# Performance work log

Measured on AMD Instinct MI355X. Metric: run time of the kernel, lower is better.

## Reference

```python
import jax, jax.numpy as jnp
import numpy as np
from jax import lax

FACTOR = 2  # downsample factor


def make_resample_kernel(k):
    k = np.asarray(k, dtype=np.float32)
    if k.ndim == 1:
        k = np.outer(k, k)
    k /= k.sum()
    return jnp.asarray(k)


def setup_inputs() -> dict:
    key = jax.random.key(0)
    x = jax.random.normal(key, (16, 512, 64, 64), dtype=jnp.float32)
    kernel = make_resample_kernel([1, 3, 3, 1])  # (4, 4), normalized binomial FIR
    return {"x": x, "kernel": kernel}


def reference(x, kernel):
    # upfirdn2d(x, kernel, up=1, down=factor, pad=((kh-factor+1)//2, (kh-factor)//2))
    # = pad -> correlate with flipped kernel (i.e. true convolution) -> stride-`factor` subsample.
    # Fused here as a single depthwise strided conv.
    n, c, h, w = x.shape
    kh, kw = kernel.shape
    pad = kh - FACTOR
    pad0, pad1 = (pad + 1) // 2, pad // 2
    wk = jnp.flip(kernel, (0, 1))[None, None]          # (1, 1, kh, kw)
    wk = jnp.broadcast_to(wk, (c, 1, kh, kw))          # depthwise kernel
    out = lax.conv_general_dilated(
        x, wk,
        window_strides=(FACTOR, FACTOR),
        padding=((pad0, pad1), (pad0, pad1)),
        dimension_numbers=("NCHW", "OIHW", "NCHW"),
        feature_group_count=c,
    )  # (n, c, h//FACTOR, w//FACTOR)
    return out
```

## Files before the change

### kernel.cpp

```cpp
#include <hip/hip_runtime.h>


#define IH 64
#define IW 64
#define OHN 32
#define OWN 32
#define HP 33

__global__ __launch_bounds__(256) void upfirdn_down2_kernel(
    const float* __restrict__ x, const float* __restrict__ kk,
    float* __restrict__ out)
{
    __shared__ float hbuf[IH * HP];

    const int t = threadIdx.x;
    const int img = blockIdx.x;
    const float* __restrict__ xi = x + (size_t)img * (IH * IW);
    float* __restrict__ oi = out + (size_t)img * (OHN * OWN);

    float km[16];
#pragma unroll
    for (int i = 0; i < 16; ++i) km[i] = kk[i];
    const float kh0 = km[3] + km[7] + km[11] + km[15];
    const float kh1 = km[2] + km[6] + km[10] + km[14];
    const float kh2 = km[1] + km[5] + km[9]  + km[13];
    const float kh3 = km[0] + km[4] + km[8]  + km[12];
    const float kv0 = km[12] + km[13] + km[14] + km[15];
    const float kv1 = km[8]  + km[9]  + km[10] + km[11];
    const float kv2 = km[4]  + km[5]  + km[6]  + km[7];
    const float kv3 = km[0]  + km[1]  + km[2]  + km[3];

    {
        const int y = t >> 2;
        const int q = t & 3;
        const float* row = xi + y * IW + q * 16;
        const float4 a0 = ((const float4*)row)[0];
        const float4 a1 = ((const float4*)row)[1];
        const float4 a2 = ((const float4*)row)[2];
        const float4 a3 = ((const float4*)row)[3];
        const float left  = (q > 0) ? row[-1] : 0.0f;
        const float right = (q < 3) ? row[16] : 0.0f;

        float v[18];
        v[0] = left;
        v[1] = a0.x;  v[2] = a0.y;  v[3] = a0.z;  v[4] = a0.w;
        v[5] = a1.x;  v[6] = a1.y;  v[7] = a1.z;  v[8] = a1.w;
        v[9] = a2.x;  v[10] = a2.y; v[11] = a2.z; v[12] = a2.w;
        v[13] = a3.x; v[14] = a3.y; v[15] = a3.z; v[16] = a3.w;
        v[17] = right;

        float* hb = &hbuf[y * HP + q * 8];
#pragma unroll
        for (int m = 0; m < 8; ++m) {
            hb[m] = kh0 * v[2 * m] + kh1 * v[2 * m + 1]
                  + kh2 * v[2 * m + 2] + kh3 * v[2 * m + 3];
        }
    }
    __syncthreads();

    {
        const int ow = t & 31;
        const int g = t >> 5;
        const int ybase = 8 * g - 1;
        float hr[10];
#pragma unroll
        for (int r = 0; r < 10; ++r) {
            const int yy = ybase + r;
            hr[r] = (yy >= 0 && yy < IH) ? hbuf[yy * HP + ow] : 0.0f;
        }
#pragma unroll
        for (int m = 0; m < 4; ++m) {
            const float o = kv0 * hr[2 * m] + kv1 * hr[2 * m + 1]
                          + kv2 * hr[2 * m + 2] + kv3 * hr[2 * m + 3];
            oi[(4 * g + m) * OWN + ow] = o;
        }
    }
}

extern "C" void kernel_launch(void* const* d_in, const int* in_sizes, int n_in,
                              void* d_out, int out_size, void* d_ws, size_t ws_size,
                              hipStream_t stream) {
    const float* x = (const float*)d_in[0];
    const float* k = (const float*)d_in[1];
    float* out = (float*)d_out;
    const int n_img = in_sizes[0] / (IH * IW);
    upfirdn_down2_kernel<<<n_img, 256, 0, stream>>>(x, k, out);
}
```

Baseline: 196.2 us.

## Coalesce input loads with lane shuffles and vectorize LDS and output accesses

Each thread now loads one float4 per iteration in a fully coalesced pattern, taking its left and right neighbours from adjacent lanes with shuffles instead of issuing separate scalar loads. The horizontal-pass buffer gains zero-padded top and bottom rows and a 36-float pitch, so the vertical pass can read four float4 rows from LDS without bounds checks and write float4 outputs. The aim is to cut uncoalesced global loads and scalar LDS and store traffic in this memory-bound kernel. Relying on shuffles assumes 16-lane row groups stay inside a wavefront, and the new pitch may change LDS bank-conflict behaviour.

Result: no change. 196.9 us (+0.3%).

```diff
diff --git a/kernel.cpp b/kernel.cpp
--- a/kernel.cpp
+++ b/kernel.cpp
@@ -5,75 +5,66 @@
 #define IW 64
 #define OHN 32
 #define OWN 32
-#define HP 33
+#define HP 36
+#define HROWS 66
 
 __global__ __launch_bounds__(256) void upfirdn_down2_kernel(
     const float* __restrict__ x, const float* __restrict__ kk,
     float* __restrict__ out)
 {
-    __shared__ float hbuf[IH * HP];
+    __shared__ float hbuf[HROWS * HP];
 
     const int t = threadIdx.x;
     const int img = blockIdx.x;
     const float* __restrict__ xi = x + (size_t)img * (IH * IW);
     float* __restrict__ oi = out + (size_t)img * (OHN * OWN);
 
-    float km[16];
+    if (t < HP) hbuf[t] = 0.0f;
+    else if (t < 2 * HP) hbuf[(HROWS - 1) * HP + (t - HP)] = 0.0f;
+
+    const float4 k0 = ((const float4*)kk)[0];
+    const float4 k1 = ((const float4*)kk)[1];
+    const float4 k2 = ((const float4*)kk)[2];
+    const float4 k3 = ((const float4*)kk)[3];
+    const float kh0 = k0.w + k1.w + k2.w + k3.w;
+    const float kh1 = k0.z + k1.z + k2.z + k3.z;
+    const float kh2 = k0.y + k1.y + k2.y + k3.y;
+    const float kh3 = k0.x + k1.x + k2.x + k3.x;
+    const float kv0 = k3.x + k3.y + k3.z + k3.w;
+    const float kv1 = k2.x + k2.y + k2.z + k2.w;
+    const float kv2 = k1.x + k1.y + k1.z + k1.w;
+    const float kv3 = k0.x + k0.y + k0.z + k0.w;
+
+    const int c4 = t & 15;
+    const int rb = t >> 4;
 #pragma unroll
-    for (int i = 0; i < 16; ++i) km[i] = kk[i];
-    const float kh0 = km[3] + km[7] + km[11] + km[15];
-    const float kh1 = km[2] + km[6] + km[10] + km[14];
-    const float kh2 = km[1] + km[5] + km[9]  + km[13];
-    const float kh3 = km[0] + km[4] + km[8]  + km[12];
-    const float kv0 = km[12] + km[13] + km[14] + km[15];
-    const float kv1 = km[8]  + km[9]  + km[10] + km[11];
-    const float kv2 = km[4]  + km[5]  + km[6]  + km[7];
-    const float kv3 = km[0]  + km[1]  + km[2]  + km[3];
-
-    {
-        const int y = t >> 2;
-        const int q = t & 3;
-        const float* row = xi + y * IW + q * 16;
-        const float4 a0 = ((const float4*)row)[0];
-        const float4 a1 = ((const float4*)row)[1];
-        const float4 a2 = ((const float4*)row)[2];
-        const float4 a3 = ((const float4*)row)[3];
-        const float left  = (q > 0) ? row[-1] : 0.0f;
-        const float right = (q < 3) ? row[16] : 0.0f;
-
-        float v[18];
-        v[0] = left;
-        v[1] = a0.x;  v[2] = a0.y;  v[3] = a0.z;  v[4] = a0.w;
-        v[5] = a1.x;  v[6] = a1.y;  v[7] = a1.z;  v[8] = a1.w;
-        v[9] = a2.x;  v[10] = a2.y; v[11] = a2.z; v[12] = a2.w;
-        v[13] = a3.x; v[14] = a3.y; v[15] = a3.z; v[16] = a3.w;
-        v[17] = right;
-
-        float* hb = &hbuf[y * HP + q * 8];
-#pragma unroll
-        for (int m = 0; m < 8; ++m) {
-            hb[m] = kh0 * v[2 * m] + kh1 * v[2 * m + 1]
-                  + kh2 * v[2 * m + 2] + kh3 * v[2 * m + 3];
-        }
+    for (int i = 0; i < 4; ++i) {
+        const float4 v = ((const float4*)xi)[i * 256 + t];
+        const int row = i * 16 + rb;
+        float lft = __shfl_up(v.w, 1);
+        float rgt = __shfl_down(v.x, 1);
+        if (c4 == 0)  lft = 0.0f;
+        if (c4 == 15) rgt = 0.0f;
+        const float h0 = kh0 * lft + kh1 * v.x + kh2 * v.y + kh3 * v.z;
+        const float h1 = kh0 * v.y + kh1 * v.z + kh2 * v.w + kh3 * rgt;
+        *(float2*)&hbuf[(row + 1) * HP + 2 * c4] = make_float2(h0, h1);
     }
     __syncthreads();
 
     {
-        const int ow = t & 31;
-        const int g = t >> 5;
-        const int ybase = 8 * g - 1;
-        float hr[10];
-#pragma unroll
-        for (int r = 0; r < 10; ++r) {
-            const int yy = ybase + r;
-            hr[r] = (yy >= 0 && yy < IH) ? hbuf[yy * HP + ow] : 0.0f;
-        }
-#pragma unroll
-        for (int m = 0; m < 4; ++m) {
-            const float o = kv0 * hr[2 * m] + kv1 * hr[2 * m + 1]
-                          + kv2 * hr[2 * m + 2] + kv3 * hr[2 * m + 3];
-            oi[(4 * g + m) * OWN + ow] = o;
-        }
+        const int ow4 = t & 7;
+        const int oh = t >> 3;
+        const float* hb = &hbuf[2 * oh * HP + 4 * ow4];
+        const float4 r0 = *(const float4*)(hb);
+        const float4 r1 = *(const float4*)(hb + HP);
+        const float4 r2 = *(const float4*)(hb + 2 * HP);
+        const float4 r3 = *(const float4*)(hb + 3 * HP);
+        float4 o;
+        o.x = kv0 * r0.x + kv1 * r1.x + kv2 * r2.x + kv3 * r3.x;
+        o.y = kv0 * r0.y + kv1 * r1.y + kv2 * r2.y + kv3 * r3.y;
+        o.z = kv0 * r0.z + kv1 * r1.z + kv2 * r2.z + kv3 * r3.z;
+        o.w = kv0 * r0.w + kv1 * r1.w + kv2 * r2.w + kv3 * r3.w;
+        *(float4*)&oi[oh * OWN + 4 * ow4] = o;
     }
 }
 
```
